# Performance work log

Hardware: AMD Instinct MI355X
Metric: run time of the kernel (lower is better)

## Reference

```python
import jax, jax.numpy as jnp
import numpy as np

TOKEN = 40      # half window -> token_len D = 81
STRIDE = 4
NHEAD = 9
EPS = 1e-5
NEG = -1e30


def _tokenize(x):
    # x: [B, L] -> [B, S, D] centered sliding windows, zero padded
    B, L = x.shape
    D = 2 * TOKEN + 1
    S = -(-L // STRIDE)
    xp = jnp.pad(x, ((0, 0), (TOKEN, TOKEN)))
    idx = jnp.arange(S)[:, None] * STRIDE + jnp.arange(D)[None, :]
    return xp[:, idx]


def _pe(S, D):
    pos = jnp.arange(S, dtype=jnp.float32)[:, None]
    div = jnp.exp(-jnp.log(jnp.float32(10000.0)) * jnp.arange(0, D, 2, dtype=jnp.float32) / D)
    ang = pos * div  # [S, ceil(D/2)]
    pe = jnp.zeros((S, D), dtype=jnp.float32)
    pe = pe.at[:, 0::2].set(jnp.sin(ang))
    pe = pe.at[:, 1::2].set(jnp.cos(ang[:, : D // 2]))
    return pe


def _bn(x, g, b, axes):
    # training-mode batch norm over `axes`, channels last
    m = x.mean(axes, keepdims=True)
    v = x.var(axes, keepdims=True)
    return (x - m) / jnp.sqrt(v + EPS) * g + b


def _forward(x, basel, cali_spec, Wq, Wk, Wq2, Wk2, Wv2, Cv, Wo1, Wo2,
             corr_weight, h_weight, corr_map, g1, b1, ff1_w, ff1_b, g2, b2,
             ff2_w, ff2_b, g3, b3, token_v_w, token_v_b, beta1, alpha1, alpha2,
             fc1_w, fc1_b, bnf1_g, bnf1_b, fc2_w, fc2_b, bnf2_g, bnf2_b, fc3_w, fc3_b):
    D = 2 * TOKEN + 1
    dk = D // NHEAD
    # data normalization (load_data_scale semantics)
    xm = jnp.min(x[:, 20:-20])
    xs = jnp.abs(jnp.max(x[:, 20:-20] - xm))
    xn = (x - xm) / xs
    bs = basel[:, ::STRIDE]                      # [B, S]
    tx = _tokenize(xn)                           # [B, S, D]
    B, S, _ = tx.shape
    pe = _pe(S, D)
    tx = tx + pe
    cn = (cali_spec - xm) / xs
    tc = _tokenize(cn) + pe                      # [Bc, S, D]
    Bc = tc.shape[0]

    # ---- branch 2: calibration-spectrum attention over the batch dim ----
    Q2 = jnp.einsum('bse,hed->shbd', tx, Wq2)    # [S,H,B,dk]
    K2 = jnp.einsum('bse,hed->shbd', tx, Wk2)
    V2 = jnp.einsum('bse,hed->shbd', tx, Wv2)
    cK = jnp.einsum('cse,hed->shcd', tc, Wk2)    # [S,H,Bc,dk]
    cV = jnp.einsum('cse,hed->shcd', tc, Wv2)
    Kc = jnp.concatenate([K2, cK], axis=2)       # [S,H,B+Bc,dk]
    Vc = jnp.concatenate([V2, cV], axis=2)
    sc = jnp.einsum('shbd,shkd->shbk', Q2, Kc) / jnp.sqrt(jnp.float32(dk))
    cols = jnp.arange(B + Bc)
    # banded mask: each sample sees only itself among batch columns, all cali columns
    mask = (cols[None, :] >= B) | (cols[None, :] == jnp.arange(B)[:, None])  # [B, B+Bc]
    sc = jnp.where(mask[None, None], sc, NEG)
    A2 = jax.nn.softmax(sc, axis=-1)
    h2 = jnp.einsum('shbk,shkd->bshd', A2, Vc).reshape(B, S, D) @ Wo2  # [B,S,D]

    # ---- branch 1: correlation-map-biased attention over spectral positions ----
    xh = tx + h2
    Qs = jnp.einsum('bse,hed->bhsd', xh, Wq)
    Ks = jnp.einsum('bse,hed->bhsd', xh, Wk)
    Vs = jnp.einsum('bse,hed->bhsd', xh, Wq)     # original uses Wq for V (bug preserved)
    cw = corr_weight[0]
    bias = (corr_map @ Cv) / jnp.sqrt(jnp.float32(S))  # band_num == S
    As = (1.0 - cw) * jnp.einsum('bhsd,bhtd->bhst', Qs, Ks) / jnp.sqrt(jnp.float32(dk)) + cw * bias
    As = jax.nn.softmax(As, axis=-1)
    h1 = jnp.einsum('bhst,bhtd->bshd', As, Vs).reshape(B, S, D) @ Wo1
    hw = h_weight[0]
    att = (1.0 - hw) * h1 + hw * h2

    # ---- SpectrA residual + FF (BatchNorm over channels) ----
    ma = _bn(att + tx, g1, b1, (0, 1))
    f = jax.nn.relu(ma @ ff1_w + ff1_b)
    f = _bn(f, g2, b2, (0, 1))
    f = jax.nn.relu(f @ ff2_w + ff2_b)
    res = _bn(ma + f, g3, b3, (0, 1))

    # ---- ACiNet head ----
    a = (res @ token_v_w + token_v_b) * jax.nn.softmax(res @ beta1, axis=-1)
    a = a.sum(-1)                                # [B, S]
    fea = alpha1[0] * a + alpha2[0] * bs
    h = jax.nn.relu(fea @ fc1_w + fc1_b)
    h = _bn(h, bnf1_g, bnf1_b, (0,))
    h = jax.nn.relu(h @ fc2_w + fc2_b)
    h = _bn(h, bnf2_g, bnf2_b, (0,))
    return jnp.tanh(h @ fc3_w + fc3_b)


def setup_inputs() -> dict:
    key = jax.random.key(0)
    ks = iter(jax.random.split(key, 64))
    def rn(shape, s=0.05):
        return jax.random.normal(next(ks), shape, dtype=jnp.float32) * s
    B, Bc, L = 32, 16, 2048
    D, H, dk, S, FF, FC1, FC2, Y = 81, 9, 9, 512, 256, 512, 256, 4
    f32 = jnp.float32
    return {
        'x': rn((B, L), 1.0), 'basel': rn((B, L), 1.0), 'cali_spec': rn((Bc, L), 1.0),
        'Wq': rn((H, D, dk)), 'Wk': rn((H, D, dk)), 'Wq2': rn((H, D, dk)),
        'Wk2': rn((H, D, dk)), 'Wv2': rn((H, D, dk)),
        'Cv': rn((S, S)), 'Wo1': rn((D, D)), 'Wo2': rn((D, D)),
        'corr_weight': jnp.array([0.2], dtype=f32), 'h_weight': jnp.array([0.8], dtype=f32),
        'corr_map': rn((S, S), 1.0),
        'g1': jnp.ones(D, f32), 'b1': jnp.zeros(D, f32),
        'ff1_w': rn((D, FF)), 'ff1_b': jnp.zeros(FF, f32),
        'g2': jnp.ones(FF, f32), 'b2': jnp.zeros(FF, f32),
        'ff2_w': rn((FF, D)), 'ff2_b': jnp.zeros(D, f32),
        'g3': jnp.ones(D, f32), 'b3': jnp.zeros(D, f32),
        'token_v_w': rn((D, D)), 'token_v_b': jnp.zeros(D, f32),
        'beta1': jnp.ones((D, D), f32),
        'alpha1': jnp.array([0.8], dtype=f32), 'alpha2': jnp.array([0.2], dtype=f32),
        'fc1_w': rn((S, FC1)), 'fc1_b': jnp.zeros(FC1, f32),
        'bnf1_g': jnp.ones(FC1, f32), 'bnf1_b': jnp.zeros(FC1, f32),
        'fc2_w': rn((FC1, FC2)), 'fc2_b': jnp.zeros(FC2, f32),
        'bnf2_g': jnp.ones(FC2, f32), 'bnf2_b': jnp.zeros(FC2, f32),
        'fc3_w': rn((FC2, Y)), 'fc3_b': jnp.zeros(Y, f32),
    }


def reference(x, basel, cali_spec, Wq, Wk, Wq2, Wk2, Wv2, Cv, Wo1, Wo2,
              corr_weight, h_weight, corr_map, g1, b1, ff1_w, ff1_b, g2, b2,
              ff2_w, ff2_b, g3, b3, token_v_w, token_v_b, beta1, alpha1, alpha2,
              fc1_w, fc1_b, bnf1_g, bnf1_b, fc2_w, fc2_b, bnf2_g, bnf2_b, fc3_w, fc3_b):
    return _forward(x, basel, cali_spec, Wq, Wk, Wq2, Wk2, Wv2, Cv, Wo1, Wo2,
                    corr_weight, h_weight, corr_map, g1, b1, ff1_w, ff1_b, g2, b2,
                    ff2_w, ff2_b, g3, b3, token_v_w, token_v_b, beta1, alpha1, alpha2,
                    fc1_w, fc1_b, bnf1_g, bnf1_b, fc2_w, fc2_b, bnf2_g, bnf2_b, fc3_w, fc3_b)
```

## Files before the change

### kernel.cpp

```cpp
#include <hip/hip_runtime.h>
#include <hip/hip_bf16.h>
#include <math.h>

#define EPSV 1e-5f

typedef float vf4 __attribute__((ext_vector_type(4)));


__global__ void minmax_part(const float* __restrict__ x, float* __restrict__ part) {
    __shared__ float smin[256], smax[256];
    int tid = threadIdx.x;
    float mn = 1e30f, mx = -1e30f;
    for (int i = blockIdx.x * 256 + tid; i < 32 * 2008; i += 64 * 256) {
        int b = i / 2008, c = i % 2008 + 20;
        float v = x[b * 2048 + c];
        mn = fminf(mn, v); mx = fmaxf(mx, v);
    }
    smin[tid] = mn; smax[tid] = mx; __syncthreads();
    for (int off = 128; off > 0; off >>= 1) {
        if (tid < off) { smin[tid] = fminf(smin[tid], smin[tid + off]); smax[tid] = fmaxf(smax[tid], smax[tid + off]); }
        __syncthreads();
    }
    if (tid == 0) { part[blockIdx.x] = smin[0]; part[64 + blockIdx.x] = smax[0]; }
}
// ... 25 lines not shown
    int idx = blockIdx.x * blockDim.x + threadIdx.x;
    if (idx >= 48 * 512 * 81) return;
    int d = idx % 81;
    int s = (idx / 81) % 512;
    int r = idx / (81 * 512);
    float xm = scal[0], inv_xs = 1.0f / scal[1];
    int oc = s * 4 + d - 40;
    float val = 0.0f;
    if (oc >= 0 && oc < 2048) {
        float sv = (r < 32) ? x[r * 2048 + oc] : cali[(r - 32) * 2048 + oc];
        val = (sv - xm) * inv_xs;
    }
    txall[idx] = val + pe[s * 81 + d];
}

__global__ __launch_bounds__(256) void qkv2_kernel(const float* __restrict__ txall,
                            const float* __restrict__ Wq2, const float* __restrict__ Wk2,
                            const float* __restrict__ Wv2,
                            float* __restrict__ Q2, float* __restrict__ Kc, float* __restrict__ Vc) {
    __shared__ float rows_[32 * 84];
    __shared__ float Wl[84 * 81];
    int blk = blockIdx.x;
    int t, rb;
    if (blk < 512)       { t = 0; rb = blk; }
    else if (blk < 1280) { t = 1; rb = blk - 512; }
    else                 { t = 2; rb = blk - 1280; }
    int row0 = rb * 32;
    int k = row0 >> 9;
    int s0 = row0 & 511;
    const float* W = (t == 0) ? Wq2 : (t == 1) ? Wk2 : Wv2;
    int tid = threadIdx.x;
    for (int i = tid; i < 32 * 84; i += 256) {
        int c = i % 84;
        rows_[i] = (c < 81) ? txall[(row0 + i / 84) * 81 + c] : 0.0f;
    }
    for (int i = tid; i < 84 * 81; i += 256) {
        int e = i / 81, hd = i % 81;
        int h = hd / 9, d = hd % 9;
        Wl[i] = (e < 81) ? W[h * 729 + e * 9 + d] : 0.0f;
    }
    __syncthreads();
    for (int o = tid; o < 8 * 81; o += 256) {
        int r4 = o / 81, hd = o % 81;
        const float* rp = rows_ + r4 * 4 * 84;
        float a0 = 0, a1 = 0, a2 = 0, a3 = 0;
        #pragma unroll 7
        for (int e = 0; e < 84; e += 4) {
            vf4 r0 = *(const vf4*)(rp + e);
            vf4 r1 = *(const vf4*)(rp + 84 + e);
            vf4 r2 = *(const vf4*)(rp + 168 + e);
            vf4 r3 = *(const vf4*)(rp + 252 + e);
            #pragma unroll
            for (int kk = 0; kk < 4; kk++) {
                float w = Wl[(e + kk) * 81 + hd];
                a0 += r0[kk] * w; a1 += r1[kk] * w;
                a2 += r2[kk] * w; a3 += r3[kk] * w;
            }
        }
        int h = hd / 9, d = hd % 9;
        int sb = s0 + r4 * 4;
        float av[4] = {a0, a1, a2, a3};
        #pragma unroll
        for (int j = 0; j < 4; j++) {
            int s = sb + j;
            if (t == 0)      Q2[((s * 9 + h) * 32 + k) * 9 + d] = av[j];
            else if (t == 1) Kc[((s * 9 + h) * 48 + k) * 9 + d] = av[j];
            else             Vc[((s * 9 + h) * 48 + k) * 9 + d] = av[j];
        }
    }
}

__global__ void attn2_kernel(const float* __restrict__ Q2, const float* __restrict__ Kc,
                             const float* __restrict__ Vc, float* __restrict__ tmp2) {
    int tid = blockIdx.x * blockDim.x + threadIdx.x;
    if (tid >= 512 * 9 * 32) return;
    int b = tid & 31;
    int h = (tid >> 5) % 9;
    int s = tid / 288;
    const float* q = Q2 + ((s * 9 + h) * 32 + b) * 9;
    float qr[9];
    #pragma unroll
    for (int d = 0; d < 9; d++) qr[d] = q[d] * (1.0f / 3.0f);
// ... 12 lines not shown
        float p = __expf(acc);
        l += p;
        const float* vp = Vb + k * 9;
        #pragma unroll
        for (int d = 0; d < 9; d++) outv[d] += p * vp[d];
    }
    float invl = 1.0f / l;
    float* op = tmp2 + (b * 512 + s) * 81 + h * 9;
    #pragma unroll
    for (int d = 0; d < 9; d++) op[d] = outv[d] * invl;
}

__global__ __launch_bounds__(256) void h2xh_kernel(const float* __restrict__ tmp2,
                            const float* __restrict__ Wo2, const float* __restrict__ txall,
                            float* __restrict__ h2, float* __restrict__ xh) {
    __shared__ float rows_[32 * 84];
    __shared__ float Wl[84 * 81];
    int row0 = blockIdx.x * 32;
    int tid = threadIdx.x;
    for (int i = tid; i < 32 * 84; i += 256) {
        int c = i % 84;
        rows_[i] = (c < 81) ? tmp2[(row0 + i / 84) * 81 + c] : 0.0f;
    }
    for (int i = tid; i < 84 * 81; i += 256) {
        int e = i / 81, c = i % 81;
        Wl[i] = (e < 81) ? Wo2[e * 81 + c] : 0.0f;
    }
    __syncthreads();
    for (int o = tid; o < 8 * 81; o += 256) {
        int r4 = o / 81, c = o % 81;
        const float* rp = rows_ + r4 * 4 * 84;
        float a0 = 0, a1 = 0, a2 = 0, a3 = 0;
        #pragma unroll 7
        for (int e = 0; e < 84; e += 4) {
            vf4 r0 = *(const vf4*)(rp + e);
            vf4 r1 = *(const vf4*)(rp + 84 + e);
            vf4 r2 = *(const vf4*)(rp + 168 + e);
            vf4 r3 = *(const vf4*)(rp + 252 + e);
            #pragma unroll
            for (int kk = 0; kk < 4; kk++) {
                float w = Wl[(e + kk) * 81 + c];
                a0 += r0[kk] * w; a1 += r1[kk] * w;
                a2 += r2[kk] * w; a3 += r3[kk] * w;
            }
        }
        float av[4] = {a0, a1, a2, a3};
        #pragma unroll
        for (int j = 0; j < 4; j++) {
            int idx = (row0 + r4 * 4 + j) * 81 + c;
            h2[idx] = av[j];
            xh[idx] = txall[idx] + av[j];
        }
    }
}

__global__ __launch_bounds__(256) void qks_kernel(const float* __restrict__ xh,
                           const float* __restrict__ Wq, const float* __restrict__ Wk,
                           float* __restrict__ Qs, float* __restrict__ Ks) {
    __shared__ float rows_[32 * 84];
    __shared__ float Wl[84 * 81];
    int blk = blockIdx.x;
    int t = blk >> 9;
    int rb = blk & 511;
    int row0 = rb * 32;
    int b = row0 >> 9;
    int s0 = row0 & 511;
    const float* W = (t == 0) ? Wq : Wk;
    int tid = threadIdx.x;
    for (int i = tid; i < 32 * 84; i += 256) {
        int c = i % 84;
        rows_[i] = (c < 81) ? xh[(row0 + i / 84) * 81 + c] : 0.0f;
    }
    for (int i = tid; i < 84 * 81; i += 256) {
        int e = i / 81, hd = i % 81;
        int h = hd / 9, d = hd % 9;
        Wl[i] = (e < 81) ? W[h * 729 + e * 9 + d] : 0.0f;
    }
    __syncthreads();
    float* dst = (t == 0) ? Qs : Ks;
    for (int o = tid; o < 8 * 81; o += 256) {
        int r4 = o / 81, hd = o % 81;
        const float* rp = rows_ + r4 * 4 * 84;
        float a0 = 0, a1 = 0, a2 = 0, a3 = 0;
        #pragma unroll 7
        for (int e = 0; e < 84; e += 4) {
            vf4 r0 = *(const vf4*)(rp + e);
            vf4 r1 = *(const vf4*)(rp + 84 + e);
            vf4 r2 = *(const vf4*)(rp + 168 + e);
            vf4 r3 = *(const vf4*)(rp + 252 + e);
            #pragma unroll
            for (int kk = 0; kk < 4; kk++) {
                float w = Wl[(e + kk) * 81 + hd];
                a0 += r0[kk] * w; a1 += r1[kk] * w;
                a2 += r2[kk] * w; a3 += r3[kk] * w;
            }
        }
        int h = hd / 9, d = hd % 9;
        int sb = s0 + r4 * 4;
        float av[4] = {a0, a1, a2, a3};
        #pragma unroll
        for (int j = 0; j < 4; j++)
            dst[((b * 9 + h) * 512 + (sb + j)) * 9 + d] = av[j];
    }
}

__global__ __launch_bounds__(256) void biasmm_kernel(const float* __restrict__ corr,
                              const float* __restrict__ Cv, const float* __restrict__ cwp,
                              float* __restrict__ ebT) {
    __shared__ float As[32][33];
    __shared__ float Bs[32][33];
    int tx = threadIdx.x, ty = threadIdx.y;
    int tid = ty * 16 + tx;
    int t0 = blockIdx.y * 32, s0 = blockIdx.x * 32;
    float a00 = 0, a01 = 0, a10 = 0, a11 = 0;
    for (int k0 = 0; k0 < 512; k0 += 32) {
        for (int ii = tid; ii < 1024; ii += 256) {
            int r = ii >> 5, c = ii & 31;
// ... 67 lines not shown
    const float* p1 = part + 1474560 + idx;
    float L = p0[0] + p1[0];
    float invl = 1.0f / L;
    int bh = idx >> 9, q = idx & 511;
    int b = bh / 9, h = bh % 9;
    float* op = h1tmp + (b * 512 + q) * 81 + h * 9;
    #pragma unroll
    for (int d = 0; d < 9; d++)
        op[d] = (p0[(1 + d) * 147456] + p1[(1 + d) * 147456]) * invl;
}

__global__ __launch_bounds__(256) void h1o_kernel(const float* __restrict__ h1tmp,
                           const float* __restrict__ Wo1, const float* __restrict__ h2,
                           const float* __restrict__ txall, const float* __restrict__ hwp,
                           float* __restrict__ matin, float* __restrict__ st1) {
    __shared__ float rows_[32 * 84];
    __shared__ float Wl[84 * 81];
    __shared__ float ssum[81], ssq[81];
    int row0 = blockIdx.x * 32;
    int tid = threadIdx.x;
    if (tid < 81) { ssum[tid] = 0.0f; ssq[tid] = 0.0f; }
    for (int i = tid; i < 32 * 84; i += 256) {
        int c = i % 84;
        rows_[i] = (c < 81) ? h1tmp[(row0 + i / 84) * 81 + c] : 0.0f;
    }
    for (int i = tid; i < 84 * 81; i += 256) {
        int e = i / 81, c = i % 81;
        Wl[i] = (e < 81) ? Wo1[e * 81 + c] : 0.0f;
    }
    __syncthreads();
    float hw = hwp[0];
    float onemhw = 1.0f - hw;
    for (int o = tid; o < 8 * 81; o += 256) {
        int r4 = o / 81, c = o % 81;
        const float* rp = rows_ + r4 * 4 * 84;
        float a0 = 0, a1 = 0, a2 = 0, a3 = 0;
        #pragma unroll 7
        for (int e = 0; e < 84; e += 4) {
            vf4 r0 = *(const vf4*)(rp + e);
            vf4 r1 = *(const vf4*)(rp + 84 + e);
            vf4 r2 = *(const vf4*)(rp + 168 + e);
            vf4 r3 = *(const vf4*)(rp + 252 + e);
            #pragma unroll
            for (int kk = 0; kk < 4; kk++) {
                float w = Wl[(e + kk) * 81 + c];
                a0 += r0[kk] * w; a1 += r1[kk] * w;
                a2 += r2[kk] * w; a3 += r3[kk] * w;
            }
        }
        float av[4] = {a0, a1, a2, a3};
        float ls = 0.0f, lq = 0.0f;
        #pragma unroll
        for (int j = 0; j < 4; j++) {
            int idx = (row0 + r4 * 4 + j) * 81 + c;
            float v = onemhw * av[j] + hw * h2[idx] + txall[idx];
            matin[idx] = v;
            ls += v; lq += v * v;
        }
        atomicAdd(&ssum[c], ls);
        atomicAdd(&ssq[c], lq);
    }
    __syncthreads();
    if (tid < 81) {
        atomicAdd(&st1[tid], ssum[tid]);
        atomicAdd(&st1[81 + tid], ssq[tid]);
    }
}

__global__ __launch_bounds__(256) void ff1_kernel(const float* __restrict__ matin,
                           const float* __restrict__ st1, const float* __restrict__ g1,
                           const float* __restrict__ b1, const float* __restrict__ W,
                           const float* __restrict__ bias, float* __restrict__ f1,
                           float* __restrict__ st2) {
    __shared__ float rows_[32 * 84];
    __shared__ float Wl[84 * 64];
    __shared__ float s2s[64], s2q[64];
    int row0 = blockIdx.x * 32;
    int c0 = blockIdx.y * 64;
    int tid = threadIdx.x;
    const float invN = 1.0f / 16384.0f;
    if (tid < 64) { s2s[tid] = 0.0f; s2q[tid] = 0.0f; }
    for (int i = tid; i < 32 * 84; i += 256) {
        int c = i % 84;
        float v = 0.0f;
        if (c < 81) {
            float mean = st1[c] * invN;
            float var = st1[81 + c] * invN - mean * mean;
            v = (matin[(row0 + i / 84) * 81 + c] - mean) * rsqrtf(var + EPSV) * g1[c] + b1[c];
        }
        rows_[i] = v;
    }
    for (int i = tid; i < 84 * 64; i += 256) {
        int e = i >> 6, cc = i & 63;
        Wl[i] = (e < 81) ? W[e * 256 + c0 + cc] : 0.0f;
    }
    __syncthreads();
    for (int o = tid; o < 8 * 64; o += 256) {
        int r4 = o >> 6, cc = o & 63;
        const float* rp = rows_ + r4 * 4 * 84;
        float a0 = 0, a1 = 0, a2 = 0, a3 = 0;
        #pragma unroll 7
        for (int e = 0; e < 84; e += 4) {
            vf4 r0 = *(const vf4*)(rp + e);
            vf4 r1 = *(const vf4*)(rp + 84 + e);
            vf4 r2 = *(const vf4*)(rp + 168 + e);
            vf4 r3 = *(const vf4*)(rp + 252 + e);
            #pragma unroll
            for (int kk = 0; kk < 4; kk++) {
                float w = Wl[((e + kk) << 6) + cc];
                a0 += r0[kk] * w; a1 += r1[kk] * w;
                a2 += r2[kk] * w; a3 += r3[kk] * w;
            }
        }
        float bv = bias[c0 + cc];
        a0 = fmaxf(a0 + bv, 0.0f); a1 = fmaxf(a1 + bv, 0.0f);
        a2 = fmaxf(a2 + bv, 0.0f); a3 = fmaxf(a3 + bv, 0.0f);
        int base = (row0 + r4 * 4) * 256 + c0 + cc;
        f1[base]       = a0;
        f1[base + 256] = a1;
        f1[base + 512] = a2;
        f1[base + 768] = a3;
        atomicAdd(&s2s[cc], a0 + a1 + a2 + a3);
        atomicAdd(&s2q[cc], a0 * a0 + a1 * a1 + a2 * a2 + a3 * a3);
    }
    __syncthreads();
    if (tid < 64) {
        atomicAdd(&st2[c0 + tid], s2s[tid]);
        atomicAdd(&st2[256 + c0 + tid], s2q[tid]);
    }
}

__global__ __launch_bounds__(256) void ff2_kernel(const float* __restrict__ f1,
                           const float* __restrict__ st2, const float* __restrict__ g2,
                           const float* __restrict__ b2, const float* __restrict__ W,
                           const float* __restrict__ bias, const float* __restrict__ matin,
                           const float* __restrict__ st1, const float* __restrict__ g1,
                           const float* __restrict__ b1, float* __restrict__ t3,
                           float* __restrict__ st3) {
    __shared__ float rows_[16 * 64];
    __shared__ float Wl[64 * 81];
    __shared__ float s3s[81], s3q[81];
    int row0 = blockIdx.x * 16;
    int tid = threadIdx.x;
    const float invN = 1.0f / 16384.0f;
    if (tid < 81) { s3s[tid] = 0.0f; s3q[tid] = 0.0f; }
    float acc[2][4];
    #pragma unroll
    for (int oi = 0; oi < 2; oi++) {
        #pragma unroll
        for (int j = 0; j < 4; j++) acc[oi][j] = 0.0f;
    }
    for (int kq = 0; kq < 4; kq++) {
        __syncthreads();
        for (int i = tid; i < 16 * 64; i += 256) {
            int r = i >> 6, e = i & 63;
            int c = kq * 64 + e;
            float mean = st2[c] * invN;
            float var = st2[256 + c] * invN - mean * mean;
            rows_[i] = (f1[(row0 + r) * 256 + c] - mean) * rsqrtf(var + EPSV) * g2[c] + b2[c];
        }
        for (int i = tid; i < 64 * 81; i += 256) {
            Wl[i] = W[(kq * 64 + i / 81) * 81 + i % 81];
        }
        __syncthreads();
        #pragma unroll
        for (int oi = 0; oi < 2; oi++) {
            int o = tid + oi * 256;
            if (o < 324) {
                int r4 = o / 81, c = o % 81;
                const float* rp = rows_ + r4 * 4 * 64;
                #pragma unroll 4
                for (int e = 0; e < 64; e += 4) {
                    vf4 r0 = *(const vf4*)(rp + e);
                    vf4 r1 = *(const vf4*)(rp + 64 + e);
                    vf4 r2 = *(const vf4*)(rp + 128 + e);
                    vf4 r3 = *(const vf4*)(rp + 192 + e);
                    #pragma unroll
                    for (int kk = 0; kk < 4; kk++) {
                        float w = Wl[(e + kk) * 81 + c];
                        acc[oi][0] += r0[kk] * w; acc[oi][1] += r1[kk] * w;
                        acc[oi][2] += r2[kk] * w; acc[oi][3] += r3[kk] * w;
                    }
                }
            }
        }
    }
    #pragma unroll
    for (int oi = 0; oi < 2; oi++) {
        int o = tid + oi * 256;
        if (o < 324) {
            int r4 = o / 81, c = o % 81;
            float mean = st1[c] * invN;
            float var = st1[81 + c] * invN - mean * mean;
            float rstd = rsqrtf(var + EPSV);
            float bval = bias[c];
            float ls = 0.0f, lq = 0.0f;
            #pragma unroll
            for (int j = 0; j < 4; j++) {
                int idx = (row0 + r4 * 4 + j) * 81 + c;
                float ma = (matin[idx] - mean) * rstd * g1[c] + b1[c];
                float v = ma + fmaxf(acc[oi][j] + bval, 0.0f);
                t3[idx] = v;
                ls += v; lq += v * v;
            }
            atomicAdd(&s3s[c], ls);
            atomicAdd(&s3q[c], lq);
        }
    }
    __syncthreads();
    if (tid < 81) {
        atomicAdd(&st3[tid], s3s[tid]);
        atomicAdd(&st3[81 + tid], s3q[tid]);
    }
}

__global__ __launch_bounds__(256) void token_kernel(const float* __restrict__ t3,
                             const float* __restrict__ st3, const float* __restrict__ g3,
                             const float* __restrict__ b3, const float* __restrict__ tvw,
                             const float* __restrict__ tvb, const float* __restrict__ beta1,
                             const float* __restrict__ basel, const float* __restrict__ a1p,
                             const float* __restrict__ a2p, float* __restrict__ fea) {
    __shared__ float rows_[32 * 81];
    __shared__ float Wu[6561];
    __shared__ float Wv[6561];
    int row0 = blockIdx.x * 32;
    int tid = threadIdx.x;
    const float invN = 1.0f / 16384.0f;
    for (int i = tid; i < 32 * 81; i += 256) {
        int c = i % 81;
        float mean = st3[c] * invN;
        float var = st3[81 + c] * invN - mean * mean;
        rows_[i] = (t3[row0 * 81 + i] - mean) * rsqrtf(var + EPSV) * g3[c] + b3[c];
    }
    for (int i = tid; i < 6561; i += 256) { Wu[i] = tvw[i]; Wv[i] = beta1[i]; }
    __syncthreads();
    int r = tid >> 3, j = tid & 7;
    const float* rp = rows_ + r * 81;
    float u[11], v[11];
    #pragma unroll
    for (int dd = 0; dd < 11; dd++) {
        int d = j + dd * 8;
        u[dd] = (d < 81) ? tvb[d] : 0.0f;
        v[dd] = (d < 81) ? 0.0f : -1e30f;
    }
    for (int e = 0; e < 81; e++) {
        float rv = rp[e];
        #pragma unroll
        for (int dd = 0; dd < 11; dd++) {
            int d = j + dd * 8;
            if (d < 81) {
                u[dd] += rv * Wu[e * 81 + d];
                v[dd] += rv * Wv[e * 81 + d];
            }
        }
    }
    float mx = -1e30f;
    #pragma unroll
    for (int dd = 0; dd < 11; dd++) mx = fmaxf(mx, v[dd]);
    #pragma unroll
    for (int msk = 1; msk < 8; msk <<= 1) mx = fmaxf(mx, __shfl_xor(mx, msk, 8));
    float sp = 0.0f, sup = 0.0f;
    #pragma unroll
    for (int dd = 0; dd < 11; dd++) {
        float p = __expf(v[dd] - mx);
        sp += p; sup += u[dd] * p;
    }
    #pragma unroll
    for (int msk = 1; msk < 8; msk <<= 1) {
        sp  += __shfl_xor(sp, msk, 8);
        sup += __shfl_xor(sup, msk, 8);
    }
    if (j == 0) {
        int rg = row0 + r;
        int b = rg >> 9, s = rg & 511;
        fea[rg] = a1p[0] * (sup / sp) + a2p[0] * basel[b * 2048 + s * 4];
    }
}

__global__ void fc1_kernel(const float* __restrict__ in, const float* __restrict__ W,
                           const float* __restrict__ bias, float* __restrict__ out,
                           float* __restrict__ st) {
    int idx = blockIdx.x * blockDim.x + threadIdx.x;
    if (idx >= 32 * 512) return;
    int b = idx >> 9, j = idx & 511;
    float acc = bias[j];
    const float* ip = in + (b << 9);
    #pragma unroll 8
    for (int k = 0; k < 512; k++) acc += ip[k] * W[k * 512 + j];
    acc = fmaxf(acc, 0.0f);
    out[idx] = acc;
// ... 131 lines not shown
    float* txall = ws + TX;
    float* Q2    = ws + Q2O;
    float* Kc    = ws + KCO;
    float* Vc    = ws + VCO;
    float* tmp2  = ws + TMP2;
    float* h2    = ws + H2O;
    float* xh    = ws + XHO;
    float* ebT   = ws + BIASO;
    float* f1    = ws + F1O;
    float* h1tmp = Q2;
    float* Qs    = Kc;
    float* Ks    = Vc;
    float* matin = tmp2;
    float* t3    = h2;
    float* apart = f1;

    hipMemsetAsync(ws, 0, 4096 * sizeof(float), stream);

    minmax_part<<<64, 256, 0, stream>>>(x, part);
    minmax_fin<<<1, 64, 0, stream>>>(part, scal);

    pe_kernel<<<(512 * 81 + 255) / 256, 256, 0, stream>>>(pe);

    tokenize_kernel<<<(48 * 512 * 81 + 255) / 256, 256, 0, stream>>>(x, cali, scal, pe, txall);

    qkv2_kernel<<<2048, 256, 0, stream>>>(txall, Wq2, Wk2, Wv2, Q2, Kc, Vc);

    attn2_kernel<<<(512 * 9 * 32) / 256, 256, 0, stream>>>(Q2, Kc, Vc, tmp2);

    h2xh_kernel<<<512, 256, 0, stream>>>(tmp2, Wo2, txall, h2, xh);

    qks_kernel<<<1024, 256, 0, stream>>>(xh, Wq, Wk, Qs, Ks);

    biasmm_kernel<<<dim3(16, 16), dim3(16, 16), 0, stream>>>(corr, Cv, corr_w, ebT);

    attn1_kernel<<<1152, 256, 0, stream>>>(Qs, Ks, ebT, corr_w, apart);
    attn1_merge<<<576, 256, 0, stream>>>(apart, h1tmp);

    h1o_kernel<<<512, 256, 0, stream>>>(h1tmp, Wo1, h2, txall, h_w, matin, st1);

    ff1_kernel<<<dim3(512, 4), 256, 0, stream>>>(matin, st1, g1, b1, ff1_w, ff1_b, f1, st2);

    ff2_kernel<<<1024, 256, 0, stream>>>(f1, st2, g2, b2, ff2_w, ff2_b,
                                         matin, st1, g1, b1, t3, st3);

    token_kernel<<<512, 256, 0, stream>>>(t3, st3, g3, b3, tvw, tvb, beta1, basel, a1, a2, fea);

    fc1_kernel<<<64, 256, 0, stream>>>(fea, fc1_w, fc1_b, fch1, st4);

    fc2_kernel<<<32, 256, 0, stream>>>(fch1, st4, bnf1_g, bnf1_b, fc2_w, fc2_b, fch2, st5);

    fc3_kernel<<<1, 128, 0, stream>>>(fch2, st5, bnf2_g, bnf2_b, fc3_w, fc3_b, out);
}
```

Measured before the change: 498.0 us.

## Use 4x4 register tiles with vectorized weight loads and split token kernel

All the small 81-wide matmul kernels now have each thread compute a 4-row by 4-column register tile. Weight tiles are padded to 84 columns so they can be read with vector loads, and each block handles 64 rows instead of 32, so half as many blocks are launched. The token kernel is split into a tiled matmul kernel that writes the u and v projections to scratch buffers, followed by a pooling kernel that does the softmax-weighted reduction. This cuts shared-memory load traffic per FMA and improves weight reuse, at the cost of more registers per thread, fewer blocks, and an extra global round trip for the token projections.

New measurement: 483.9 us. 1.03x faster.

```diff
diff --git a/kernel.cpp b/kernel.cpp
--- a/kernel.cpp
+++ b/kernel.cpp
@@ -63,58 +63,66 @@
     txall[idx] = val + pe[s * 81 + d];
 }
 
+
 __global__ __launch_bounds__(256) void qkv2_kernel(const float* __restrict__ txall,
                             const float* __restrict__ Wq2, const float* __restrict__ Wk2,
                             const float* __restrict__ Wv2,
                             float* __restrict__ Q2, float* __restrict__ Kc, float* __restrict__ Vc) {
-    __shared__ float rows_[32 * 84];
-    __shared__ float Wl[84 * 81];
+    __shared__ float rows_[64 * 84];
+    __shared__ float Wl[84 * 84];
     int blk = blockIdx.x;
     int t, rb;
-    if (blk < 512)       { t = 0; rb = blk; }
-    else if (blk < 1280) { t = 1; rb = blk - 512; }
-    else                 { t = 2; rb = blk - 1280; }
-    int row0 = rb * 32;
+    if (blk < 256)      { t = 0; rb = blk; }
+    else if (blk < 640) { t = 1; rb = blk - 256; }
+    else                { t = 2; rb = blk - 640; }
+    int row0 = rb * 64;
     int k = row0 >> 9;
     int s0 = row0 & 511;
     const float* W = (t == 0) ? Wq2 : (t == 1) ? Wk2 : Wv2;
     int tid = threadIdx.x;
-    for (int i = tid; i < 32 * 84; i += 256) {
+    for (int i = tid; i < 64 * 84; i += 256) {
         int c = i % 84;
         rows_[i] = (c < 81) ? txall[(row0 + i / 84) * 81 + c] : 0.0f;
     }
-    for (int i = tid; i < 84 * 81; i += 256) {
-        int e = i / 81, hd = i % 81;
-        int h = hd / 9, d = hd % 9;
-        Wl[i] = (e < 81) ? W[h * 729 + e * 9 + d] : 0.0f;
-    }
-    __syncthreads();
-    for (int o = tid; o < 8 * 81; o += 256) {
-        int r4 = o / 81, hd = o % 81;
+    for (int i = tid; i < 84 * 84; i += 256) {
+        int e = i / 84, hd = i % 84;
+        Wl[i] = (e < 81 && hd < 81) ? W[(hd / 9) * 729 + e * 9 + (hd % 9)] : 0.0f;
+    }
+    __syncthreads();
+    for (int o = tid; o < 336; o += 256) {
+        int r4 = o / 21, cg = o % 21;
+        int c0 = cg * 4;
         const float* rp = rows_ + r4 * 4 * 84;
-        float a0 = 0, a1 = 0, a2 = 0, a3 = 0;
+        vf4 acc0 = 0.0f, acc1 = 0.0f, acc2 = 0.0f, acc3 = 0.0f;
         #pragma unroll 7
         for (int e = 0; e < 84; e += 4) {
+            vf4 w0 = *(const vf4*)(Wl + (e + 0) * 84 + c0);
+            vf4 w1 = *(const vf4*)(Wl + (e + 1) * 84 + c0);
+            vf4 w2 = *(const vf4*)(Wl + (e + 2) * 84 + c0);
+            vf4 w3 = *(const vf4*)(Wl + (e + 3) * 84 + c0);
             vf4 r0 = *(const vf4*)(rp + e);
             vf4 r1 = *(const vf4*)(rp + 84 + e);
             vf4 r2 = *(const vf4*)(rp + 168 + e);
             vf4 r3 = *(const vf4*)(rp + 252 + e);
-            #pragma unroll
-            for (int kk = 0; kk < 4; kk++) {
-                float w = Wl[(e + kk) * 81 + hd];
-                a0 += r0[kk] * w; a1 += r1[kk] * w;
-                a2 += r2[kk] * w; a3 += r3[kk] * w;
+            acc0 += r0[0] * w0 + r0[1] * w1 + r0[2] * w2 + r0[3] * w3;
+            acc1 += r1[0] * w0 + r1[1] * w1 + r1[2] * w2 + r1[3] * w3;
+            acc2 += r2[0] * w0 + r2[1] * w1 + r2[2] * w2 + r2[3] * w3;
+            acc3 += r3[0] * w0 + r3[1] * w1 + r3[2] * w2 + r3[3] * w3;
+        }
+        vf4 av[4] = {acc0, acc1, acc2, acc3};
+        #pragma unroll
+        for (int cc = 0; cc < 4; cc++) {
+            int col = c0 + cc;
+            if (col < 81) {
+                int h = col / 9, d = col % 9;
+                #pragma unroll
+                for (int rr = 0; rr < 4; rr++) {
+                    int s = s0 + r4 * 4 + rr;
+                    if (t == 0)      Q2[((s * 9 + h) * 32 + k) * 9 + d] = av[rr][cc];
+                    else if (t == 1) Kc[((s * 9 + h) * 48 + k) * 9 + d] = av[rr][cc];
+                    else             Vc[((s * 9 + h) * 48 + k) * 9 + d] = av[rr][cc];
+                }
             }
-        }
-        int h = hd / 9, d = hd % 9;
-        int sb = s0 + r4 * 4;
-        float av[4] = {a0, a1, a2, a3};
-        #pragma unroll
-        for (int j = 0; j < 4; j++) {
-            int s = sb + j;
-            if (t == 0)      Q2[((s * 9 + h) * 32 + k) * 9 + d] = av[j];
-            else if (t == 1) Kc[((s * 9 + h) * 48 + k) * 9 + d] = av[j];
-            else             Vc[((s * 9 + h) * 48 + k) * 9 + d] = av[j];
         }
     }
 }
@@ -157,42 +165,52 @@
 __global__ __launch_bounds__(256) void h2xh_kernel(const float* __restrict__ tmp2,
                             const float* __restrict__ Wo2, const float* __restrict__ txall,
                             float* __restrict__ h2, float* __restrict__ xh) {
-    __shared__ float rows_[32 * 84];
-    __shared__ float Wl[84 * 81];
-    int row0 = blockIdx.x * 32;
-    int tid = threadIdx.x;
-    for (int i = tid; i < 32 * 84; i += 256) {
+    __shared__ float rows_[64 * 84];
+    __shared__ float Wl[84 * 84];
+    int row0 = blockIdx.x * 64;
+    int tid = threadIdx.x;
+    for (int i = tid; i < 64 * 84; i += 256) {
         int c = i % 84;
         rows_[i] = (c < 81) ? tmp2[(row0 + i / 84) * 81 + c] : 0.0f;
     }
-    for (int i = tid; i < 84 * 81; i += 256) {
-        int e = i / 81, c = i % 81;
-        Wl[i] = (e < 81) ? Wo2[e * 81 + c] : 0.0f;
-    }
-    __syncthreads();
-    for (int o = tid; o < 8 * 81; o += 256) {
-        int r4 = o / 81, c = o % 81;
+    for (int i = tid; i < 84 * 84; i += 256) {
+        int e = i / 84, c = i % 84;
+        Wl[i] = (e < 81 && c < 81) ? Wo2[e * 81 + c] : 0.0f;
+    }
+    __syncthreads();
+    for (int o = tid; o < 336; o += 256) {
+        int r4 = o / 21, cg = o % 21;
+        int c0 = cg * 4;
         const float* rp = rows_ + r4 * 4 * 84;
-        float a0 = 0, a1 = 0, a2 = 0, a3 = 0;
+        vf4 acc0 = 0.0f, acc1 = 0.0f, acc2 = 0.0f, acc3 = 0.0f;
         #pragma unroll 7
         for (int e = 0; e < 84; e += 4) {
+            vf4 w0 = *(const vf4*)(Wl + (e + 0) * 84 + c0);
+            vf4 w1 = *(const vf4*)(Wl + (e + 1) * 84 + c0);
+            vf4 w2 = *(const vf4*)(Wl + (e + 2) * 84 + c0);
+            vf4 w3 = *(const vf4*)(Wl + (e + 3) * 84 + c0);
             vf4 r0 = *(const vf4*)(rp + e);
             vf4 r1 = *(const vf4*)(rp + 84 + e);
             vf4 r2 = *(const vf4*)(rp + 168 + e);
             vf4 r3 = *(const vf4*)(rp + 252 + e);
-            #pragma unroll
-            for (int kk = 0; kk < 4; kk++) {
-                float w = Wl[(e + kk) * 81 + c];
-                a0 += r0[kk] * w; a1 += r1[kk] * w;
-                a2 += r2[kk] * w; a3 += r3[kk] * w;
+            acc0 += r0[0] * w0 + r0[1] * w1 + r0[2] * w2 + r0[3] * w3;
+            acc1 += r1[0] * w0 + r1[1] * w1 + r1[2] * w2 + r1[3] * w3;
+            acc2 += r2[0] * w0 + r2[1] * w1 + r2[2] * w2 + r2[3] * w3;
+            acc3 += r3[0] * w0 + r3[1] * w1 + r3[2] * w2 + r3[3] * w3;
+        }
+        vf4 av[4] = {acc0, acc1, acc2, acc3};
+        #pragma unroll
+        for (int cc = 0; cc < 4; cc++) {
+            int col = c0 + cc;
+            if (col < 81) {
+                #pragma unroll
+                for (int rr = 0; rr < 4; rr++) {
+                    int idx = (row0 + r4 * 4 + rr) * 81 + col;
+                    float v = av[rr][cc];
+                    h2[idx] = v;
+                    xh[idx] = txall[idx] + v;
+                }
             }
-        }
-        float av[4] = {a0, a1, a2, a3};
-        #pragma unroll
-        for (int j = 0; j < 4; j++) {
-            int idx = (row0 + r4 * 4 + j) * 81 + c;
-            h2[idx] = av[j];
-            xh[idx] = txall[idx] + av[j];
         }
     }
 }
@@ -200,50 +218,57 @@
 __global__ __launch_bounds__(256) void qks_kernel(const float* __restrict__ xh,
                            const float* __restrict__ Wq, const float* __restrict__ Wk,
                            float* __restrict__ Qs, float* __restrict__ Ks) {
-    __shared__ float rows_[32 * 84];
-    __shared__ float Wl[84 * 81];
+    __shared__ float rows_[64 * 84];
+    __shared__ float Wl[84 * 84];
     int blk = blockIdx.x;
-    int t = blk >> 9;
-    int rb = blk & 511;
-    int row0 = rb * 32;
+    int t = blk >> 8;
+    int rb = blk & 255;
+    int row0 = rb * 64;
     int b = row0 >> 9;
     int s0 = row0 & 511;
     const float* W = (t == 0) ? Wq : Wk;
     int tid = threadIdx.x;
-    for (int i = tid; i < 32 * 84; i += 256) {
+    for (int i = tid; i < 64 * 84; i += 256) {
         int c = i % 84;
         rows_[i] = (c < 81) ? xh[(row0 + i / 84) * 81 + c] : 0.0f;
     }
-    for (int i = tid; i < 84 * 81; i += 256) {
-        int e = i / 81, hd = i % 81;
-        int h = hd / 9, d = hd % 9;
-        Wl[i] = (e < 81) ? W[h * 729 + e * 9 + d] : 0.0f;
+    for (int i = tid; i < 84 * 84; i += 256) {
+        int e = i / 84, hd = i % 84;
+        Wl[i] = (e < 81 && hd < 81) ? W[(hd / 9) * 729 + e * 9 + (hd % 9)] : 0.0f;
     }
     __syncthreads();
     float* dst = (t == 0) ? Qs : Ks;
-    for (int o = tid; o < 8 * 81; o += 256) {
-        int r4 = o / 81, hd = o % 81;
+    for (int o = tid; o < 336; o += 256) {
+        int r4 = o / 21, cg = o % 21;
+        int c0 = cg * 4;
         const float* rp = rows_ + r4 * 4 * 84;
-        float a0 = 0, a1 = 0, a2 = 0, a3 = 0;
+        vf4 acc0 = 0.0f, acc1 = 0.0f, acc2 = 0.0f, acc3 = 0.0f;
         #pragma unroll 7
         for (int e = 0; e < 84; e += 4) {
+            vf4 w0 = *(const vf4*)(Wl + (e + 0) * 84 + c0);
+            vf4 w1 = *(const vf4*)(Wl + (e + 1) * 84 + c0);
+            vf4 w2 = *(const vf4*)(Wl + (e + 2) * 84 + c0);
+            vf4 w3 = *(const vf4*)(Wl + (e + 3) * 84 + c0);
             vf4 r0 = *(const vf4*)(rp + e);
             vf4 r1 = *(const vf4*)(rp + 84 + e);
             vf4 r2 = *(const vf4*)(rp + 168 + e);
             vf4 r3 = *(const vf4*)(rp + 252 + e);
-            #pragma unroll
-            for (int kk = 0; kk < 4; kk++) {
-                float w = Wl[(e + kk) * 81 + hd];
-                a0 += r0[kk] * w; a1 += r1[kk] * w;
-                a2 += r2[kk] * w; a3 += r3[kk] * w;
+            acc0 += r0[0] * w0 + r0[1] * w1 + r0[2] * w2 + r0[3] * w3;
+            acc1 += r1[0] * w0 + r1[1] * w1 + r1[2] * w2 + r1[3] * w3;
+            acc2 += r2[0] * w0 + r2[1] * w1 + r2[2] * w2 + r2[3] * w3;
+            acc3 += r3[0] * w0 + r3[1] * w1 + r3[2] * w2 + r3[3] * w3;
+        }
+        vf4 av[4] = {acc0, acc1, acc2, acc3};
+        #pragma unroll
+        for (int cc = 0; cc < 4; cc++) {
+            int col = c0 + cc;
+            if (col < 81) {
+                int h = col / 9, d = col % 9;
+                #pragma unroll
+                for (int rr = 0; rr < 4; rr++)
+                    dst[((b * 9 + h) * 512 + (s0 + r4 * 4 + rr)) * 9 + d] = av[rr][cc];
             }
         }
-        int h = hd / 9, d = hd % 9;
-        int sb = s0 + r4 * 4;
-        float av[4] = {a0, a1, a2, a3};
-        #pragma unroll
-        for (int j = 0; j < 4; j++)
-            dst[((b * 9 + h) * 512 + (sb + j)) * 9 + d] = av[j];
     }
 }
 
@@ -341,51 +366,60 @@
                            const float* __restrict__ Wo1, const float* __restrict__ h2,
                            const float* __restrict__ txall, const float* __restrict__ hwp,
                            float* __restrict__ matin, float* __restrict__ st1) {
-    __shared__ float rows_[32 * 84];
-    __shared__ float Wl[84 * 81];
+    __shared__ float rows_[64 * 84];
+    __shared__ float Wl[84 * 84];
     __shared__ float ssum[81], ssq[81];
-    int row0 = blockIdx.x * 32;
+    int row0 = blockIdx.x * 64;
     int tid = threadIdx.x;
     if (tid < 81) { ssum[tid] = 0.0f; ssq[tid] = 0.0f; }
-    for (int i = tid; i < 32 * 84; i += 256) {
+    for (int i = tid; i < 64 * 84; i += 256) {
         int c = i % 84;
         rows_[i] = (c < 81) ? h1tmp[(row0 + i / 84) * 81 + c] : 0.0f;
     }
-    for (int i = tid; i < 84 * 81; i += 256) {
-        int e = i / 81, c = i % 81;
-        Wl[i] = (e < 81) ? Wo1[e * 81 + c] : 0.0f;
+    for (int i = tid; i < 84 * 84; i += 256) {
+        int e = i / 84, c = i % 84;
+        Wl[i] = (e < 81 && c < 81) ? Wo1[e * 81 + c] : 0.0f;
     }
     __syncthreads();
     float hw = hwp[0];
     float onemhw = 1.0f - hw;
-    for (int o = tid; o < 8 * 81; o += 256) {
-        int r4 = o / 81, c = o % 81;
+    for (int o = tid; o < 336; o += 256) {
+        int r4 = o / 21, cg = o % 21;
+        int c0 = cg * 4;
         const float* rp = rows_ + r4 * 4 * 84;
-        float a0 = 0, a1 = 0, a2 = 0, a3 = 0;
+        vf4 acc0 = 0.0f, acc1 = 0.0f, acc2 = 0.0f, acc3 = 0.0f;
         #pragma unroll 7
         for (int e = 0; e < 84; e += 4) {
+            vf4 w0 = *(const vf4*)(Wl + (e + 0) * 84 + c0);
+            vf4 w1 = *(const vf4*)(Wl + (e + 1) * 84 + c0);
+            vf4 w2 = *(const vf4*)(Wl + (e + 2) * 84 + c0);
+            vf4 w3 = *(const vf4*)(Wl + (e + 3) * 84 + c0);
             vf4 r0 = *(const vf4*)(rp + e);
             vf4 r1 = *(const vf4*)(rp + 84 + e);
             vf4 r2 = *(const vf4*)(rp + 168 + e);
             vf4 r3 = *(const vf4*)(rp + 252 + e);
-            #pragma unroll
-            for (int kk = 0; kk < 4; kk++) {
-                float w = Wl[(e + kk) * 81 + c];
-                a0 += r0[kk] * w; a1 += r1[kk] * w;
-                a2 += r2[kk] * w; a3 += r3[kk] * w;
+            acc0 += r0[0] * w0 + r0[1] * w1 + r0[2] * w2 + r0[3] * w3;
+            acc1 += r1[0] * w0 + r1[1] * w1 + r1[2] * w2 + r1[3] * w3;
+            acc2 += r2[0] * w0 + r2[1] * w1 + r2[2] * w2 + r2[3] * w3;
+            acc3 += r3[0] * w0 + r3[1] * w1 + r3[2] * w2 + r3[3] * w3;
+        }
+        vf4 av[4] = {acc0, acc1, acc2, acc3};
+        #pragma unroll
+        for (int cc = 0; cc < 4; cc++) {
+            int col = c0 + cc;
+            if (col < 81) {
+                float ls = 0.0f, lq = 0.0f;
+                #pragma unroll
+                for (int rr = 0; rr < 4; rr++) {
+                    int idx = (row0 + r4 * 4 + rr) * 81 + col;
+                    float v = onemhw * av[rr][cc] + hw * h2[idx] + txall[idx];
+                    matin[idx] = v;
+                    ls += v; lq += v * v;
+                }
+                atomicAdd(&ssum[col], ls);
+                atomicAdd(&ssq[col], lq);
             }
         }
-        float av[4] = {a0, a1, a2, a3};
-        float ls = 0.0f, lq = 0.0f;
-        #pragma unroll
-        for (int j = 0; j < 4; j++) {
-            int idx = (row0 + r4 * 4 + j) * 81 + c;
-            float v = onemhw * av[j] + hw * h2[idx] + txall[idx];
-            matin[idx] = v;
-            ls += v; lq += v * v;
-        }
-        atomicAdd(&ssum[c], ls);
-        atomicAdd(&ssq[c], lq);
     }
     __syncthreads();
     if (tid < 81) {
@@ -399,15 +433,15 @@
                            const float* __restrict__ b1, const float* __restrict__ W,
                            const float* __restrict__ bias, float* __restrict__ f1,
                            float* __restrict__ st2) {
-    __shared__ float rows_[32 * 84];
+    __shared__ float rows_[64 * 84];
     __shared__ float Wl[84 * 64];
     __shared__ float s2s[64], s2q[64];
-    int row0 = blockIdx.x * 32;
-    int c0 = blockIdx.y * 64;
+    int row0 = blockIdx.x * 64;
+    int cb = blockIdx.y * 64;
     int tid = threadIdx.x;
     const float invN = 1.0f / 16384.0f;
     if (tid < 64) { s2s[tid] = 0.0f; s2q[tid] = 0.0f; }
-    for (int i = tid; i < 32 * 84; i += 256) {
+    for (int i = tid; i < 64 * 84; i += 256) {
         int c = i % 84;
         float v = 0.0f;
         if (c < 81) {
@@ -419,41 +453,52 @@
     }
     for (int i = tid; i < 84 * 64; i += 256) {
         int e = i >> 6, cc = i & 63;
-        Wl[i] = (e < 81) ? W[e * 256 + c0 + cc] : 0.0f;
-    }
-    __syncthreads();
-    for (int o = tid; o < 8 * 64; o += 256) {
-        int r4 = o >> 6, cc = o & 63;
+        Wl[i] = (e < 81) ? W[e * 256 + cb + cc] : 0.0f;
+    }
+    __syncthreads();
+    {
+        int o = tid;
+        int r4 = o >> 4, cg = o & 15;
+        int c0 = cg * 4;
         const float* rp = rows_ + r4 * 4 * 84;
-        float a0 = 0, a1 = 0, a2 = 0, a3 = 0;
+        vf4 acc0 = 0.0f, acc1 = 0.0f, acc2 = 0.0f, acc3 = 0.0f;
         #pragma unroll 7
         for (int e = 0; e < 84; e += 4) {
+            vf4 w0 = *(const vf4*)(Wl + ((e + 0) << 6) + c0);
+            vf4 w1 = *(const vf4*)(Wl + ((e + 1) << 6) + c0);
+            vf4 w2 = *(const vf4*)(Wl + ((e + 2) << 6) + c0);
+            vf4 w3 = *(const vf4*)(Wl + ((e + 3) << 6) + c0);
             vf4 r0 = *(const vf4*)(rp + e);
             vf4 r1 = *(const vf4*)(rp + 84 + e);
             vf4 r2 = *(const vf4*)(rp + 168 + e);
             vf4 r3 = *(const vf4*)(rp + 252 + e);
-            #pragma unroll
-            for (int kk = 0; kk < 4; kk++) {
-                float w = Wl[((e + kk) << 6) + cc];
-                a0 += r0[kk] * w; a1 += r1[kk] * w;
-                a2 += r2[kk] * w; a3 += r3[kk] * w;
-            }
-        }
-        float bv = bias[c0 + cc];
-        a0 = fmaxf(a0 + bv, 0.0f); a1 = fmaxf(a1 + bv, 0.0f);
-        a2 = fmaxf(a2 + bv, 0.0f); a3 = fmaxf(a3 + bv, 0.0f);
-        int base = (row0 + r4 * 4) * 256 + c0 + cc;
-        f1[base]       = a0;
-        f1[base + 256] = a1;
-        f1[base + 512] = a2;
-        f1[base + 768] = a3;
-        atomicAdd(&s2s[cc], a0 + a1 + a2 + a3);
-        atomicAdd(&s2q[cc], a0 * a0 + a1 * a1 + a2 * a2 + a3 * a3);
+            acc0 += r0[0] * w0 + r0[1] * w1 + r0[2] * w2 + r0[3] * w3;
+            acc1 += r1[0] * w0 + r1[1] * w1 + r1[2] * w2 + r1[3] * w3;
+            acc2 += r2[0] * w0 + r2[1] * w1 + r2[2] * w2 + r2[3] * w3;
+            acc3 += r3[0] * w0 + r3[1] * w1 + r3[2] * w2 + r3[3] * w3;
+        }
+        vf4 bv = *(const vf4*)(bias + cb + c0);
+        acc0 = __builtin_elementwise_max(acc0 + bv, (vf4)0.0f);
+        acc1 = __builtin_elementwise_max(acc1 + bv, (vf4)0.0f);
+        acc2 = __builtin_elementwise_max(acc2 + bv, (vf4)0.0f);
+        acc3 = __builtin_elementwise_max(acc3 + bv, (vf4)0.0f);
+        int base = (row0 + r4 * 4) * 256 + cb + c0;
+        *(vf4*)(f1 + base)       = acc0;
+        *(vf4*)(f1 + base + 256) = acc1;
+        *(vf4*)(f1 + base + 512) = acc2;
+        *(vf4*)(f1 + base + 768) = acc3;
+        vf4 cs = acc0 + acc1 + acc2 + acc3;
+        vf4 cq = acc0 * acc0 + acc1 * acc1 + acc2 * acc2 + acc3 * acc3;
+        #pragma unroll
+        for (int cc = 0; cc < 4; cc++) {
+            atomicAdd(&s2s[c0 + cc], cs[cc]);
+            atomicAdd(&s2q[c0 + cc], cq[cc]);
+        }
     }
     __syncthreads();
     if (tid < 64) {
-        atomicAdd(&st2[c0 + tid], s2s[tid]);
-        atomicAdd(&st2[256 + c0 + tid], s2q[tid]);
+        atomicAdd(&st2[cb + tid], s2s[tid]);
+        atomicAdd(&st2[256 + cb + tid], s2q[tid]);
     }
 }
 
@@ -464,74 +509,73 @@
                            const float* __restrict__ st1, const float* __restrict__ g1,
                            const float* __restrict__ b1, float* __restrict__ t3,
                            float* __restrict__ st3) {
-    __shared__ float rows_[16 * 64];
-    __shared__ float Wl[64 * 81];
+    __shared__ float rows_[32 * 64];
+    __shared__ float Wl[64 * 84];
     __shared__ float s3s[81], s3q[81];
-    int row0 = blockIdx.x * 16;
+    int row0 = blockIdx.x * 32;
     int tid = threadIdx.x;
     const float invN = 1.0f / 16384.0f;
     if (tid < 81) { s3s[tid] = 0.0f; s3q[tid] = 0.0f; }
-    float acc[2][4];
-    #pragma unroll
-    for (int oi = 0; oi < 2; oi++) {
-        #pragma unroll
-        for (int j = 0; j < 4; j++) acc[oi][j] = 0.0f;
-    }
+    int o = tid;
+    int r4 = o / 21, cg = o % 21;
+    int c0 = cg * 4;
+    bool active = (o < 168);
+    vf4 acc0 = 0.0f, acc1 = 0.0f, acc2 = 0.0f, acc3 = 0.0f;
     for (int kq = 0; kq < 4; kq++) {
         __syncthreads();
-        for (int i = tid; i < 16 * 64; i += 256) {
+        for (int i = tid; i < 32 * 64; i += 256) {
             int r = i >> 6, e = i & 63;
             int c = kq * 64 + e;
             float mean = st2[c] * invN;
             float var = st2[256 + c] * invN - mean * mean;
             rows_[i] = (f1[(row0 + r) * 256 + c] - mean) * rsqrtf(var + EPSV) * g2[c] + b2[c];
         }
-        for (int i = tid; i < 64 * 81; i += 256) {
-            Wl[i] = W[(kq * 64 + i / 81) * 81 + i % 81];
+        for (int i = tid; i < 64 * 84; i += 256) {
+            int e = i / 84, c = i % 84;
+            Wl[i] = (c < 81) ? W[(kq * 64 + e) * 81 + c] : 0.0f;
         }
         __syncthreads();
-        #pragma unroll
-        for (int oi = 0; oi < 2; oi++) {
-            int o = tid + oi * 256;
-            if (o < 324) {
-                int r4 = o / 81, c = o % 81;
-                const float* rp = rows_ + r4 * 4 * 64;
-                #pragma unroll 4
-                for (int e = 0; e < 64; e += 4) {
-                    vf4 r0 = *(const vf4*)(rp + e);
-                    vf4 r1 = *(const vf4*)(rp + 64 + e);
-                    vf4 r2 = *(const vf4*)(rp + 128 + e);
-                    vf4 r3 = *(const vf4*)(rp + 192 + e);
-                    #pragma unroll
-                    for (int kk = 0; kk < 4; kk++) {
-                        float w = Wl[(e + kk) * 81 + c];
-                        acc[oi][0] += r0[kk] * w; acc[oi][1] += r1[kk] * w;
-                        acc[oi][2] += r2[kk] * w; acc[oi][3] += r3[kk] * w;
-                    }
+        if (active) {
+            const float* rp = rows_ + r4 * 4 * 64;
+            #pragma unroll 8
+            for (int e = 0; e < 64; e += 4) {
+                vf4 w0 = *(const vf4*)(Wl + (e + 0) * 84 + c0);
+                vf4 w1 = *(const vf4*)(Wl + (e + 1) * 84 + c0);
+                vf4 w2 = *(const vf4*)(Wl + (e + 2) * 84 + c0);
+                vf4 w3 = *(const vf4*)(Wl + (e + 3) * 84 + c0);
+                vf4 r0 = *(const vf4*)(rp + e);
+                vf4 r1 = *(const vf4*)(rp + 64 + e);
+                vf4 r2 = *(const vf4*)(rp + 128 + e);
+                vf4 r3 = *(const vf4*)(rp + 192 + e);
+                acc0 += r0[0] * w0 + r0[1] * w1 + r0[2] * w2 + r0[3] * w3;
+                acc1 += r1[0] * w0 + r1[1] * w1 + r1[2] * w2 + r1[3] * w3;
+                acc2 += r2[0] * w0 + r2[1] * w1 + r2[2] * w2 + r2[3] * w3;
+                acc3 += r3[0] * w0 + r3[1] * w1 + r3[2] * w2 + r3[3] * w3;
+            }
+        }
+    }
+    if (active) {
+        vf4 av[4] = {acc0, acc1, acc2, acc3};
+        #pragma unroll
+        for (int cc = 0; cc < 4; cc++) {
+            int col = c0 + cc;
+            if (col < 81) {
+                float mean = st1[col] * invN;
+                float var = st1[81 + col] * invN - mean * mean;
+                float rstd = rsqrtf(var + EPSV);
+                float bval = bias[col];
+                float ls = 0.0f, lq = 0.0f;
+                #pragma unroll
+                for (int rr = 0; rr < 4; rr++) {
+                    int idx = (row0 + r4 * 4 + rr) * 81 + col;
+                    float ma = (matin[idx] - mean) * rstd * g1[col] + b1[col];
+                    float v = ma + fmaxf(av[rr][cc] + bval, 0.0f);
+                    t3[idx] = v;
+                    ls += v; lq += v * v;
                 }
+                atomicAdd(&s3s[col], ls);
+                atomicAdd(&s3q[col], lq);
             }
-        }
-    }
-    #pragma unroll
-    for (int oi = 0; oi < 2; oi++) {
-        int o = tid + oi * 256;
-        if (o < 324) {
-            int r4 = o / 81, c = o % 81;
-            float mean = st1[c] * invN;
-            float var = st1[81 + c] * invN - mean * mean;
-            float rstd = rsqrtf(var + EPSV);
-            float bval = bias[c];
-            float ls = 0.0f, lq = 0.0f;
-            #pragma unroll
-            for (int j = 0; j < 4; j++) {
-                int idx = (row0 + r4 * 4 + j) * 81 + c;
-                float ma = (matin[idx] - mean) * rstd * g1[c] + b1[c];
-                float v = ma + fmaxf(acc[oi][j] + bval, 0.0f);
-                t3[idx] = v;
-                ls += v; lq += v * v;
-            }
-            atomicAdd(&s3s[c], ls);
-            atomicAdd(&s3q[c], lq);
         }
     }
     __syncthreads();
@@ -541,44 +585,85 @@
     }
 }
 
-__global__ __launch_bounds__(256) void token_kernel(const float* __restrict__ t3,
-                             const float* __restrict__ st3, const float* __restrict__ g3,
-                             const float* __restrict__ b3, const float* __restrict__ tvw,
-                             const float* __restrict__ tvb, const float* __restrict__ beta1,
+__global__ __launch_bounds__(256) void token_mm(const float* __restrict__ t3,
+                            const float* __restrict__ st3, const float* __restrict__ g3,
+                            const float* __restrict__ b3, const float* __restrict__ tvw,
+                            const float* __restrict__ beta1,
+                            float* __restrict__ uv0, float* __restrict__ uv1) {
+    __shared__ float rows_[64 * 84];
+    __shared__ float Wl[84 * 84];
+    int blk = blockIdx.x;
+    int t = blk >> 8;
+    int row0 = (blk & 255) * 64;
+    const float* W = (t == 0) ? tvw : beta1;
+    float* dst = (t == 0) ? uv0 : uv1;
+    int tid = threadIdx.x;
+    const float invN = 1.0f / 16384.0f;
+    for (int i = tid; i < 64 * 84; i += 256) {
+        int c = i % 84;
+        float v = 0.0f;
+        if (c < 81) {
+            float mean = st3[c] * invN;
+            float var = st3[81 + c] * invN - mean * mean;
+            v = (t3[(row0 + i / 84) * 81 + c] - mean) * rsqrtf(var + EPSV) * g3[c] + b3[c];
+        }
+        rows_[i] = v;
+    }
+    for (int i = tid; i < 84 * 84; i += 256) {
+        int e = i / 84, c = i % 84;
+        Wl[i] = (e < 81 && c < 81) ? W[e * 81 + c] : 0.0f;
+    }
+    __syncthreads();
+    for (int o = tid; o < 336; o += 256) {
+        int r4 = o / 21, cg = o % 21;
+        int c0 = cg * 4;
+        const float* rp = rows_ + r4 * 4 * 84;
+        vf4 acc0 = 0.0f, acc1 = 0.0f, acc2 = 0.0f, acc3 = 0.0f;
+        #pragma unroll 7
+        for (int e = 0; e < 84; e += 4) {
+            vf4 w0 = *(const vf4*)(Wl + (e + 0) * 84 + c0);
+            vf4 w1 = *(const vf4*)(Wl + (e + 1) * 84 + c0);
+            vf4 w2 = *(const vf4*)(Wl + (e + 2) * 84 + c0);
+            vf4 w3 = *(const vf4*)(Wl + (e + 3) * 84 + c0);
+            vf4 r0 = *(const vf4*)(rp + e);
+            vf4 r1 = *(const vf4*)(rp + 84 + e);
+            vf4 r2 = *(const vf4*)(rp + 168 + e);
+            vf4 r3 = *(const vf4*)(rp + 252 + e);
+            acc0 += r0[0] * w0 + r0[1] * w1 + r0[2] * w2 + r0[3] * w3;
+            acc1 += r1[0] * w0 + r1[1] * w1 + r1[2] * w2 + r1[3] * w3;
+            acc2 += r2[0] * w0 + r2[1] * w1 + r2[2] * w2 + r2[3] * w3;
+            acc3 += r3[0] * w0 + r3[1] * w1 + r3[2] * w2 + r3[3] * w3;
+        }
+        vf4 av[4] = {acc0, acc1, acc2, acc3};
+        #pragma unroll
+        for (int cc = 0; cc < 4; cc++) {
+            int col = c0 + cc;
+            if (col < 81) {
+                #pragma unroll
+                for (int rr = 0; rr < 4; rr++)
+                    dst[(row0 + r4 * 4 + rr) * 81 + col] = av[rr][cc];
+            }
+        }
+    }
+}
+
+__global__ __launch_bounds__(256) void token_pool(const float* __restrict__ uv0,
+                             const float* __restrict__ uv1, const float* __restrict__ tvb,
                              const float* __restrict__ basel, const float* __restrict__ a1p,
                              const float* __restrict__ a2p, float* __restrict__ fea) {
-    __shared__ float rows_[32 * 81];
-    __shared__ float Wu[6561];
-    __shared__ float Wv[6561];
-    int row0 = blockIdx.x * 32;
-    int tid = threadIdx.x;
-    const float invN = 1.0f / 16384.0f;
-    for (int i = tid; i < 32 * 81; i += 256) {
-        int c = i % 81;
-        float mean = st3[c] * invN;
-        float var = st3[81 + c] * invN - mean * mean;
-        rows_[i] = (t3[row0 * 81 + i] - mean) * rsqrtf(var + EPSV) * g3[c] + b3[c];
-    }
-    for (int i = tid; i < 6561; i += 256) { Wu[i] = tvw[i]; Wv[i] = beta1[i]; }
-    __syncthreads();
+    int tid = threadIdx.x;
     int r = tid >> 3, j = tid & 7;
-    const float* rp = rows_ + r * 81;
+    int row = blockIdx.x * 32 + r;
+    int base = row * 81;
     float u[11], v[11];
     #pragma unroll
     for (int dd = 0; dd < 11; dd++) {
         int d = j + dd * 8;
-        u[dd] = (d < 81) ? tvb[d] : 0.0f;
-        v[dd] = (d < 81) ? 0.0f : -1e30f;
-    }
-    for (int e = 0; e < 81; e++) {
-        float rv = rp[e];
-        #pragma unroll
-        for (int dd = 0; dd < 11; dd++) {
-            int d = j + dd * 8;
-            if (d < 81) {
-                u[dd] += rv * Wu[e * 81 + d];
-                v[dd] += rv * Wv[e * 81 + d];
-            }
+        if (d < 81) {
+            u[dd] = uv0[base + d] + tvb[d];
+            v[dd] = uv1[base + d];
+        } else {
+            u[dd] = 0.0f; v[dd] = -1e30f;
         }
     }
     float mx = -1e30f;
@@ -598,9 +683,8 @@
         sup += __shfl_xor(sup, msk, 8);
     }
     if (j == 0) {
-        int rg = row0 + r;
-        int b = rg >> 9, s = rg & 511;
-        fea[rg] = a1p[0] * (sup / sp) + a2p[0] * basel[b * 2048 + s * 4];
+        int b = row >> 9, s = row & 511;
+        fea[row] = a1p[0] * (sup / sp) + a2p[0] * basel[b * 2048 + s * 4];
     }
 }
 
@@ -762,6 +846,8 @@
     float* matin = tmp2;
     float* t3    = h2;
     float* apart = f1;
+    float* uv0   = tmp2;
+    float* uv1   = xh;
 
     hipMemsetAsync(ws, 0, 4096 * sizeof(float), stream);
 
@@ -772,27 +858,28 @@
 
     tokenize_kernel<<<(48 * 512 * 81 + 255) / 256, 256, 0, stream>>>(x, cali, scal, pe, txall);
 
-    qkv2_kernel<<<2048, 256, 0, stream>>>(txall, Wq2, Wk2, Wv2, Q2, Kc, Vc);
+    qkv2_kernel<<<1024, 256, 0, stream>>>(txall, Wq2, Wk2, Wv2, Q2, Kc, Vc);
 
     attn2_kernel<<<(512 * 9 * 32) / 256, 256, 0, stream>>>(Q2, Kc, Vc, tmp2);
 
-    h2xh_kernel<<<512, 256, 0, stream>>>(tmp2, Wo2, txall, h2, xh);
-
-    qks_kernel<<<1024, 256, 0, stream>>>(xh, Wq, Wk, Qs, Ks);
+    h2xh_kernel<<<256, 256, 0, stream>>>(tmp2, Wo2, txall, h2, xh);
+
+    qks_kernel<<<512, 256, 0, stream>>>(xh, Wq, Wk, Qs, Ks);
 
     biasmm_kernel<<<dim3(16, 16), dim3(16, 16), 0, stream>>>(corr, Cv, corr_w, ebT);
 
     attn1_kernel<<<1152, 256, 0, stream>>>(Qs, Ks, ebT, corr_w, apart);
     attn1_merge<<<576, 256, 0, stream>>>(apart, h1tmp);
 
-    h1o_kernel<<<512, 256, 0, stream>>>(h1tmp, Wo1, h2, txall, h_w, matin, st1);
-
-    ff1_kernel<<<dim3(512, 4), 256, 0, stream>>>(matin, st1, g1, b1, ff1_w, ff1_b, f1, st2);
-
-    ff2_kernel<<<1024, 256, 0, stream>>>(f1, st2, g2, b2, ff2_w, ff2_b,
-                                         matin, st1, g1, b1, t3, st3);
-
-    token_kernel<<<512, 256, 0, stream>>>(t3, st3, g3, b3, tvw, tvb, beta1, basel, a1, a2, fea);
+    h1o_kernel<<<256, 256, 0, stream>>>(h1tmp, Wo1, h2, txall, h_w, matin, st1);
+
+    ff1_kernel<<<dim3(256, 4), 256, 0, stream>>>(matin, st1, g1, b1, ff1_w, ff1_b, f1, st2);
+
+    ff2_kernel<<<512, 256, 0, stream>>>(f1, st2, g2, b2, ff2_w, ff2_b,
+                                        matin, st1, g1, b1, t3, st3);
+
+    token_mm<<<512, 256, 0, stream>>>(t3, st3, g3, b3, tvw, beta1, uv0, uv1);
+    token_pool<<<512, 256, 0, stream>>>(uv0, uv1, tvb, basel, a1, a2, fea);
 
     fc1_kernel<<<64, 256, 0, stream>>>(fea, fc1_w, fc1_b, fch1, st4);
 
```
